# Performance work log

Measured on AMD Instinct MI355X. Metric: run time of the kernel, lower is better.

## Reference

```python
import jax, jax.numpy as jnp
import numpy as np

N, E, IN, H0, H1 = 50000, 1600000, 64, 64, 128


def _gcn(h, W, b, row, col):
    # PyG GCNConv, add_self_loops=False, unit edge weights:
    # out[col] += d^{-1/2}[row] * d^{-1/2}[col] * (h @ W)[row]; bias added after aggregation
    n = h.shape[0]
    deg = jnp.zeros((n,), h.dtype).at[col].add(jnp.ones((row.shape[0],), h.dtype))
    dinv = jnp.where(deg > 0, jax.lax.rsqrt(jnp.maximum(deg, 1e-12)), 0.0)
    norm = (dinv[row] * dinv[col])[:, None]  # [E,1]
    m = h @ W  # transform before propagate (small GEMM)
    out = jnp.zeros((n, W.shape[1]), h.dtype).at[col].add(norm * m[row])
    return out + b


def _bn(h, g, b):
    # BatchNorm1d training-mode math (biased variance), eps=1e-5
    mu = h.mean(0)
    var = ((h - mu) ** 2).mean(0)
    return g * (h - mu) * jax.lax.rsqrt(var + 1e-5) + b


def _san(h):
    return jnp.nan_to_num(h, nan=0.0, posinf=100.0, neginf=-100.0)


def _slice(x, ei, W0, b0, W1, b1, res1, g0, be0, g1, be1):
    row, col = ei[0], ei[1]
    # layer 0: conv -> bn -> relu -> (dropout=eval identity) -> residual (Identity, 64==64) -> nan_to_num
    h1 = _san(jax.nn.relu(_bn(_gcn(x, W0, b0, row, col), g0, be0)) + x)
    # layer 1 (last): conv -> bn -> residual (Linear proj 64->128, no bias) -> nan_to_num
    h2 = _san(_bn(_gcn(h1, W1, b1, row, col), g1, be1) + h1 @ res1)
    return h2


def setup_inputs() -> dict:
    k = jax.random.split(jax.random.key(0), 16)
    f = lambda kk, sh, s: jax.random.normal(kk, sh, jnp.float32) * s
    return {
        "x": f(k[0], (N, IN), 1.0),
        "edge_index0": jax.random.randint(k[1], (2, E), 0, N),
        "edge_index1": jax.random.randint(k[2], (2, E), 0, N),
        "w0_s0": f(k[3], (IN, H0), 0.1), "b0_s0": jnp.zeros((H0,), jnp.float32),
        "w1_s0": f(k[4], (H0, H1), 0.1), "b1_s0": jnp.zeros((H1,), jnp.float32),
        "res1_s0": f(k[5], (H0, H1), 0.1),
        "w0_s1": f(k[6], (IN, H0), 0.1), "b0_s1": jnp.zeros((H0,), jnp.float32),
        "w1_s1": f(k[7], (H0, H1), 0.1), "b1_s1": jnp.zeros((H1,), jnp.float32),
        "res1_s1": f(k[8], (H0, H1), 0.1),
        "bn_g0": jnp.ones((H0,), jnp.float32), "bn_b0": jnp.zeros((H0,), jnp.float32),
        "bn_g1": jnp.ones((H1,), jnp.float32), "bn_b1": jnp.zeros((H1,), jnp.float32),
        "fc1_w": f(k[9], (2 * H1, H1), 0.1), "fc1_b": jnp.zeros((H1,), jnp.float32),
        "fc2_w": f(k[10], (H1, 2), 0.1), "fc2_b": jnp.zeros((2,), jnp.float32),
    }


def reference(x, edge_index0, edge_index1,
              w0_s0, b0_s0, w1_s0, b1_s0, res1_s0,
              w0_s1, b0_s1, w1_s1, b1_s1, res1_s1,
              bn_g0, bn_b0, bn_g1, bn_b1,
              fc1_w, fc1_b, fc2_w, fc2_b):
    out0 = _slice(x, edge_index0, w0_s0, b0_s0, w1_s0, b1_s0, res1_s0, bn_g0, bn_b0, bn_g1, bn_b1)
    out1 = _slice(x, edge_index1, w0_s1, b0_s1, w1_s1, b1_s1, res1_s1, bn_g0, bn_b0, bn_g1, bn_b1)
    combined = jnp.concatenate([out0, out1], axis=1)  # [N, 2*H1]
    h = jax.nn.relu(combined @ fc1_w + fc1_b)  # dropout is eval-mode identity
    logits = h @ fc2_w + fc2_b
    return logits, jax.nn.softmax(logits, axis=1)
```

## Files before the change

kernel.cpp:

```cpp
#include <hip/hip_runtime.h>
#include <hip/hip_bf16.h>
#include <math.h>


typedef short v8s __attribute__((ext_vector_type(8)));
typedef float f32x4 __attribute__((ext_vector_type(4)));

#define BSTRIDE 10240

__device__ __forceinline__ float sanf(float v) {
    if (v != v) return 0.f;
    if (isinf(v)) return v > 0.f ? 100.f : -100.f;
    return v;
}

__device__ __forceinline__ unsigned short bf16of(float v) {
    __hip_bfloat16 h = __float2bfloat16(v);
    return *(unsigned short*)&h;
}
__device__ __forceinline__ unsigned pack2(float lo, float hi) {
    return (unsigned)bf16of(lo) | ((unsigned)bf16of(hi) << 16);
}
__device__ __forceinline__ float uflo(unsigned u) { return __uint_as_float(u << 16); }
__device__ __forceinline__ float ufhi(unsigned u) { return __uint_as_float(u & 0xFFFF0000u); }
__device__ __forceinline__ float fofbf16(unsigned short u) {
    return __uint_as_float(((unsigned)u) << 16);
}

__device__ __forceinline__ void packone(const float* __restrict__ src, unsigned* __restrict__ dst,
                                        int L, int Khalf, int F) {
    int c = L / Khalf, kp = L - c * Khalf;
    dst[L] = pack2(src[(2 * kp) * F + c], src[(2 * kp + 1) * F + c]);
}

__global__ __launch_bounds__(256) void prep_kernel(const float* __restrict__ w0_0,
                                                   const float* __restrict__ w0_1,
                                                   const float* __restrict__ w1_0,
                                                   const float* __restrict__ w1_1,
                                                   const float* __restrict__ r_0,
                                                   const float* __restrict__ r_1,
                                                   const float* __restrict__ fc1,
                                                   unsigned* __restrict__ wpk,
                                                   int* __restrict__ bcnt,
                                                   float* __restrict__ sums) {
    int gid = blockIdx.x * 256 + threadIdx.x;
    if (gid < 512) bcnt[gid] = 0;
    if (gid < 8192) sums[gid] = 0.f;
    if (gid < 2048)       packone(w0_0, wpk + 0,     gid - 0,     32, 64);
    else if (gid < 4096)  packone(w0_1, wpk + 2048,  gid - 2048,  32, 64);
    else if (gid < 8192)  packone(w1_0, wpk + 4096,  gid - 4096,  32, 128);
    else if (gid < 12288) packone(w1_1, wpk + 8192,  gid - 8192,  32, 128);
    else if (gid < 16384) packone(r_0,  wpk + 12288, gid - 12288, 32, 128);
    else if (gid < 20480) packone(r_1,  wpk + 16384, gid - 16384, 32, 128);
    else if (gid < 36864) packone(fc1,  wpk + 20480, gid - 20480, 128, 128);
}


__global__ __launch_bounds__(512) void kC_bin(const int* __restrict__ ei0,
                                              const int* __restrict__ ei1,
                                              int* __restrict__ bcnt,
                                              unsigned* __restrict__ binned,
                                              int E, int n) {
    __shared__ int cnt[512];
    __shared__ int base[512];
    int t = threadIdx.x;
    cnt[t] = 0;
    int E2 = 2 * E;
    int e0 = blockIdx.x * 8192;
    unsigned pk[16];
    int bk[16];
    __syncthreads();
#pragma unroll
    for (int j = 0; j < 16; ++j) {
        int ge = e0 + t + j * 512;
        bk[j] = -1;
        if (ge < E2) {
            int slice = ge >= E;
            const int* ei = slice ? ei1 : ei0;
            int e = ge - slice * E;
            int col = ei[E + e], row = ei[e];
            int gcol = slice * n + col;
            bk[j] = gcol >> 8;
            pk[j] = (unsigned)row | (((unsigned)gcol & 255u) << 16);
            atomicAdd(&cnt[bk[j]], 1);
        }
    }
    __syncthreads();
    {
        int c = cnt[t];
        base[t] = c ? atomicAdd(&bcnt[t], c) : 0;
    }
    __syncthreads();
    cnt[t] = 0;
    __syncthreads();
#pragma unroll
    for (int j = 0; j < 16; ++j) {
        if (bk[j] >= 0) {
            int loc = atomicAdd(&cnt[bk[j]], 1);
            int off = base[bk[j]] + loc;
            if (off < BSTRIDE) binned[(size_t)bk[j] * BSTRIDE + off] = pk[j];
        }
    }
}

__global__ __launch_bounds__(256) void kB_scan(const int* __restrict__ bcnt,
                                               int* __restrict__ bstart, int NB) {
    __shared__ int tmp[256];
    int t = threadIdx.x, carry = 0;
    for (int bse = 0; bse < NB; bse += 256) {
        int i = bse + t;
        int v = (i < NB) ? bcnt[i] : 0;
        tmp[t] = v;
        __syncthreads();
        for (int off = 1; off < 256; off <<= 1) {
            int u = (t >= off) ? tmp[t - off] : 0;
            __syncthreads();
            tmp[t] += u;
            __syncthreads();
        }
        if (i < NB) bstart[i] = tmp[t] - v + carry;
        carry += tmp[255];
        __syncthreads();
    }
    if (t == 0) bstart[NB] = carry;
}

__global__ __launch_bounds__(512) void kD_build(const unsigned* __restrict__ binned,
                                                const int* __restrict__ bstart,
                                                int* __restrict__ rowptr,
                                                float* __restrict__ dinv,
                                                unsigned short* __restrict__ csr,
                                                int n2, int NB) {
    __shared__ int cnt[256];
    __shared__ int scn[256];
    __shared__ int cur[256];
    int b = blockIdx.x, t = threadIdx.x;
    int s = bstart[b], e = bstart[b + 1];
    int m = e - s;
    const unsigned* seg = binned + (size_t)b * BSTRIDE;
    if (t < 256) cnt[t] = 0;
    __syncthreads();
    for (int i = t; i < m; i += 512) atomicAdd(&cnt[(seg[i] >> 16) & 255], 1);
    __syncthreads();
    int v = (t < 256) ? cnt[t] : 0;
    if (t < 256) scn[t] = v;
    __syncthreads();
    for (int off = 1; off < 256; off <<= 1) {
        int u = (t < 256 && t >= off) ? scn[t - off] : 0;
        __syncthreads();
        if (t < 256) scn[t] += u;
        __syncthreads();
    }
    if (t < 256) {
        int excl = scn[t] - v;
        int gcol = b * 256 + t;
        if (gcol < n2) {
            rowptr[gcol] = s + excl;
            dinv[gcol] = v > 0 ? rsqrtf((float)v) : 0.f;
        }
        cur[t] = excl;
    }
    __syncthreads();
    for (int i = t; i < m; i += 512) {
        unsigned p = seg[i];
        int cl = (p >> 16) & 255;
        int pos = s + atomicAdd(&cur[cl], 1);
        csr[pos] = (unsigned short)(p & 0xFFFFu);
    }
    if (b == 0 && t == 0) rowptr[n2] = bstart[NB];
}


__global__ __launch_bounds__(256) void prescale_bf(const float* __restrict__ x,
                                                   const float* __restrict__ dinv,
                                                   unsigned short* __restrict__ xsb,
                                                   int n64, int n) {
    int i = blockIdx.x * 256 + threadIdx.x;
    if (i >= n64) return;
    int row = i >> 6;
    float v = x[i];
    xsb[i] = bf16of(v * dinv[row]);
    xsb[n64 + i] = bf16of(v * dinv[n + row]);
}

__global__ __launch_bounds__(256) void gatherbf_kernel(const int* __restrict__ rowptr,
                                                       const unsigned short* __restrict__ csr,
                                                       const unsigned short* __restrict__ m,
                                                       const float* __restrict__ dinv,
                                                       unsigned short* __restrict__ outb,
                                                       int n, int n2) {
    int gid = blockIdx.x * 256 + threadIdx.x;
    int node = gid >> 3;
    if (node >= n2) return;
    int l = threadIdx.x & 7;
    const unsigned short* mb = m + (size_t)((node >= n) ? n : 0) * 64;
    int s = rowptr[node], e = rowptr[node + 1];
    float a0 = 0.f, a1 = 0.f, a2 = 0.f, a3 = 0.f, a4 = 0.f, a5 = 0.f, a6 = 0.f, a7 = 0.f;
    int b = s;
    for (; b + 8 <= e; b += 8) {
        int idx = csr[b + l];
        uint4 u[8];
#pragma unroll
        for (int j = 0; j < 8; ++j) {
            int r = __shfl(idx, j, 8);
            u[j] = *(const uint4*)&mb[(size_t)r * 64 + l * 8];
        }
#pragma unroll
        for (int j = 0; j < 8; ++j) {
            a0 += uflo(u[j].x); a1 += ufhi(u[j].x);
            a2 += uflo(u[j].y); a3 += ufhi(u[j].y);
            a4 += uflo(u[j].z); a5 += ufhi(u[j].z);
            a6 += uflo(u[j].w); a7 += ufhi(u[j].w);
        }
    }
    if (b < e) {
        int cntn = e - b;
        int idx = (b + l < e) ? (int)csr[b + l] : 0;
        for (int j = 0; j < cntn; ++j) {
            int r = __shfl(idx, j, 8);
            uint4 u = *(const uint4*)&mb[(size_t)r * 64 + l * 8];
            a0 += uflo(u.x); a1 += ufhi(u.x);
            a2 += uflo(u.y); a3 += ufhi(u.y);
            a4 += uflo(u.z); a5 += ufhi(u.z);
            a6 += uflo(u.w); a7 += ufhi(u.w);
        }
    }
    float d = dinv[node];
    uint4 o;
    o.x = pack2(a0 * d, a1 * d);
    o.y = pack2(a2 * d, a3 * d);
    o.z = pack2(a4 * d, a5 * d);
    o.w = pack2(a6 * d, a7 * d);
    *(uint4*)&outb[(size_t)node * 64 + l * 8] = o;
}


template <int F>
__global__ __launch_bounds__(256) void mfma_gemmb(const unsigned short* __restrict__ Ab,
                                                  const unsigned* __restrict__ WT0,
                                                  const unsigned* __restrict__ WT1,
                                                  unsigned short* __restrict__ Cb,
                                                  float* __restrict__ sums_base,
                                                  int roff, int n) {
    constexpr int NC = F / 16;
    __shared__ float ls[2 * F];
    int BPS = (n + 63) >> 6;
    int slice = blockIdx.x >= BPS;
    int sb = blockIdx.x - slice * BPS;
    const unsigned* WT = slice ? WT1 : WT0;
    int row0 = slice * n + sb * 64;
    int rows = min(64, n - sb * 64);
    for (int i = threadIdx.x; i < 2 * F; i += 256) ls[i] = 0.f;
    int w = threadIdx.x >> 6, lane = threadIdx.x & 63, q = lane >> 4, ln = lane & 15;
    const unsigned* A32 = (const unsigned*)Ab;
    size_t arow = (size_t)(row0 + 16 * w + ln) * 32;
    v8s af0 = *(const v8s*)&A32[arow + q * 4];
    v8s af1 = *(const v8s*)&A32[arow + 16 + q * 4];
    f32x4 acc[NC];
#pragma unroll
    for (int ct = 0; ct < NC; ++ct) acc[ct] = {0.f, 0.f, 0.f, 0.f};
#pragma unroll
    for (int ct = 0; ct < NC; ++ct) {
        v8s b0 = *(const v8s*)&WT[(ct * 16 + ln) * 32 + q * 4];
        v8s b1 = *(const v8s*)&WT[(ct * 16 + ln) * 32 + 16 + q * 4];
        acc[ct] = __builtin_amdgcn_mfma_f32_16x16x32_bf16(af0, b0, acc[ct], 0, 0, 0);
        acc[ct] = __builtin_amdgcn_mfma_f32_16x16x32_bf16(af1, b1, acc[ct], 0, 0, 0);
    }
    __syncthreads();
#pragma unroll
    for (int ct = 0; ct < NC; ++ct) {
        float s1 = 0.f, s2 = 0.f;
#pragma unroll
        for (int i = 0; i < 4; ++i) {
            int r = 16 * w + q * 4 + i;
            if (r < rows) {
                float v = acc[ct][i];
                Cb[(size_t)(row0 + r) * F + ct * 16 + ln] = bf16of(v);
                s1 += v;
                s2 += v * v;
            }
        }
        s1 += __shfl_xor(s1, 16); s1 += __shfl_xor(s1, 32);
        s2 += __shfl_xor(s2, 16); s2 += __shfl_xor(s2, 32);
        if (q == 0) {
            atomicAdd(&ls[ct * 16 + ln], s1);
            atomicAdd(&ls[F + ct * 16 + ln], s2);
        }
    }
    __syncthreads();
    if (threadIdx.x < F) {
        float* dst = sums_base + (blockIdx.x & 7) * 1024 + roff + slice * 2 * F;
        unsafeAtomicAdd(&dst[threadIdx.x], ls[threadIdx.x]);
        unsafeAtomicAdd(&dst[F + threadIdx.x], ls[F + threadIdx.x]);
    }
}

__global__ __launch_bounds__(256) void mfma_apply1(const unsigned short* __restrict__ h1b,
                                                   const unsigned short* __restrict__ Tb,
                                                   const unsigned* __restrict__ RT0,
                                                   const unsigned* __restrict__ RT1,
                                                   const float* __restrict__ scsh,
                                                   unsigned short* __restrict__ comb, int n) {
    int BPS = (n + 63) >> 6;
    int slice = blockIdx.x >= BPS;
    int sb = blockIdx.x - slice * BPS;
    const unsigned* WT = slice ? RT1 : RT0;
    int row0 = slice * n + sb * 64;
    int rows = min(64, n - sb * 64);
    int w = threadIdx.x >> 6, lane = threadIdx.x & 63, q = lane >> 4, ln = lane & 15;
    const unsigned* A32 = (const unsigned*)h1b;
    size_t arow = (size_t)(row0 + 16 * w + ln) * 32;
    v8s af0 = *(const v8s*)&A32[arow + q * 4];
    v8s af1 = *(const v8s*)&A32[arow + 16 + q * 4];
    f32x4 acc[8];
#pragma unroll
    for (int ct = 0; ct < 8; ++ct) acc[ct] = {0.f, 0.f, 0.f, 0.f};
#pragma unroll
    for (int ct = 0; ct < 8; ++ct) {
        v8s b0 = *(const v8s*)&WT[(ct * 16 + ln) * 32 + q * 4];
        v8s b1 = *(const v8s*)&WT[(ct * 16 + ln) * 32 + 16 + q * 4];
        acc[ct] = __builtin_amdgcn_mfma_f32_16x16x32_bf16(af0, b0, acc[ct], 0, 0, 0);
        acc[ct] = __builtin_amdgcn_mfma_f32_16x16x32_bf16(af1, b1, acc[ct], 0, 0, 0);
    }
    const float* sc = scsh + slice * 256;
#pragma unroll
    for (int ct = 0; ct < 8; ++ct) {
        int c = ct * 16 + ln;
        float scale = sc[c], shift = sc[128 + c];
#pragma unroll
        for (int i = 0; i < 4; ++i) {
            int r = 16 * w + q * 4 + i;
            if (r >= rows) continue;
            int row = row0 + r;
            float tv = fofbf16(Tb[(size_t)row * 128 + c]);
            float o = sanf(fmaf(tv, scale, shift) + acc[ct][i]);
            comb[(size_t)(row - slice * n) * 256 + slice * 128 + c] = bf16of(o);
        }
    }
}

__global__ __launch_bounds__(256) void mfma_head_fc2(const unsigned short* __restrict__ comb,
                                                     const unsigned* __restrict__ FT,
                                                     const float* __restrict__ bias,
                                                     const float* __restrict__ w2,
                                                     const float* __restrict__ b2,
                                                     float* __restrict__ out, int n) {
    int row0 = blockIdx.x * 64;
    int rows = min(64, n - row0);
    int w = threadIdx.x >> 6, lane = threadIdx.x & 63, q = lane >> 4, ln = lane & 15;
    const unsigned* A32 = (const unsigned*)comb;
    size_t arow = (size_t)(row0 + 16 * w + ln) * 128;
    f32x4 acc[8];
#pragma unroll
    for (int ct = 0; ct < 8; ++ct) acc[ct] = {0.f, 0.f, 0.f, 0.f};
#pragma unroll
    for (int kt = 0; kt < 4; ++kt) {
        v8s af0 = *(const v8s*)&A32[arow + kt * 32 + q * 4];
        v8s af1 = *(const v8s*)&A32[arow + kt * 32 + 16 + q * 4];
#pragma unroll
        for (int ct = 0; ct < 8; ++ct) {
            v8s b0 = *(const v8s*)&FT[(ct * 16 + ln) * 128 + kt * 32 + q * 4];
            v8s b1 = *(const v8s*)&FT[(ct * 16 + ln) * 128 + kt * 32 + 16 + q * 4];
            acc[ct] = __builtin_amdgcn_mfma_f32_16x16x32_bf16(af0, b0, acc[ct], 0, 0, 0);
            acc[ct] = __builtin_amdgcn_mfma_f32_16x16x32_bf16(af1, b1, acc[ct], 0, 0, 0);
        }
    }
    float p0[4] = {0.f, 0.f, 0.f, 0.f}, p1[4] = {0.f, 0.f, 0.f, 0.f};
#pragma unroll
    for (int ct = 0; ct < 8; ++ct) {
        int c = ct * 16 + ln;
        float bi = bias[c];
        float w20 = w2[c * 2], w21 = w2[c * 2 + 1];
#pragma unroll
        for (int i = 0; i < 4; ++i) {
            float h = fmaxf(acc[ct][i] + bi, 0.f);
            p0[i] = fmaf(h, w20, p0[i]);
            p1[i] = fmaf(h, w21, p1[i]);
        }
    }
#pragma unroll
    for (int i = 0; i < 4; ++i) {
#pragma unroll
        for (int msk = 1; msk < 16; msk <<= 1) {
            p0[i] += __shfl_xor(p0[i], msk);
            p1[i] += __shfl_xor(p1[i], msk);
        }
    }
    if (ln == 0) {
        float bb0 = b2[0], bb1 = b2[1];
#pragma unroll
        for (int i = 0; i < 4; ++i) {
            int r = 16 * w + q * 4 + i;
            if (r >= rows) continue;
            int R = row0 + r;
            float l0 = p0[i] + bb0, l1 = p1[i] + bb1;
            float mx = fmaxf(l0, l1);
            float e0 = expf(l0 - mx), e1 = expf(l1 - mx);
            float inv = 1.0f / (e0 + e1);
            out[(size_t)R * 2] = l0;
            out[(size_t)R * 2 + 1] = l1;
            out[(size_t)2 * n + R * 2] = e0 * inv;
            out[(size_t)2 * n + R * 2 + 1] = e1 * inv;
        }
    }
}


template <int F>
__global__ void bnfinal_kernel(const float* __restrict__ sums_base, int roff,
                               const float* __restrict__ g,
                               const float* __restrict__ be, float* __restrict__ scsh, int n) {
    int f = threadIdx.x;
    if (f >= F) return;
    int slice = blockIdx.x;
    float s1 = 0.f, s2 = 0.f;
#pragma unroll
    for (int r = 0; r < 8; ++r) {
        const float* src = sums_base + r * 1024 + roff + slice * 2 * F;
        s1 += src[f];
        s2 += src[F + f];
    }
    float inv_n = 1.0f / (float)n;
    float mu = s1 * inv_n;
    float var = fmaxf(s2 * inv_n - mu * mu, 0.f);
    float scale = g[f] * rsqrtf(var + 1e-5f);
    scsh[slice * 2 * F + f] = scale;
    scsh[slice * 2 * F + F + f] = be[f] - mu * scale;
}

__global__ __launch_bounds__(256) void apply0_kernel(const unsigned short* __restrict__ t0b,
                                                     const float* __restrict__ x,
                                                     const float* __restrict__ scsh,
                                                     const float* __restrict__ dinv,
                                                     unsigned short* __restrict__ h1b,
                                                     unsigned short* __restrict__ h1sb,
                                                     int n64, int total) {
    int i = blockIdx.x * 256 + threadIdx.x;
    if (i >= total) return;
    int slice = i >= n64;
    int f = i & 63;
    const float* sc = scsh + slice * 128;
    float v = fmaf(fofbf16(t0b[i]), sc[f], sc[64 + f]);
    v = fmaxf(v, 0.f) + x[i - slice * n64];
    v = sanf(v);
    h1b[i] = bf16of(v);
    h1sb[i] = bf16of(v * dinv[i >> 6]);
}

static inline int cdiv(int a, int b) { return (a + b - 1) / b; }

extern "C" void kernel_launch(void* const* d_in, const int* in_sizes, int n_in,
                              void* d_out, int out_size, void* d_ws, size_t ws_size,
                              hipStream_t stream) {
    const float* x       = (const float*)d_in[0];
    const int*   ei0     = (const int*)d_in[1];
    const int*   ei1     = (const int*)d_in[2];
    const float* w0_s0   = (const float*)d_in[3];
    const float* w1_s0   = (const float*)d_in[5];
    const float* res1_s0 = (const float*)d_in[7];
    const float* w0_s1   = (const float*)d_in[8];
    const float* w1_s1   = (const float*)d_in[10];
    const float* res1_s1 = (const float*)d_in[12];
    const float* bn_g0   = (const float*)d_in[13];
    const float* bn_b0   = (const float*)d_in[14];
    const float* bn_g1   = (const float*)d_in[15];
    const float* bn_b1   = (const float*)d_in[16];
    const float* fc1_w   = (const float*)d_in[17];
    const float* fc1_b   = (const float*)d_in[18];
    const float* fc2_w   = (const float*)d_in[19];
    const float* fc2_b   = (const float*)d_in[20];
    float* out = (float*)d_out;

    int n = in_sizes[0] / 64;
    int E = in_sizes[1] / 2;
    int n2 = 2 * n, E2 = 2 * E;
    int n64 = n * 64;
    int NB = cdiv(n2, 256);
    int BPS = cdiv(n, 64);

    float* X1 = (float*)d_ws;
    float* S  = X1 + (size_t)n2 * 64;
    unsigned short* Gb   = (unsigned short*)(S + (size_t)n2 * 64);
    unsigned short* h1b  = Gb + (size_t)n2 * 64;
    unsigned short* comb = h1b + (size_t)n2 * 64;
    unsigned short* xsb  = comb + (size_t)n * 256;
    float* dinv = (float*)(xsb + (size_t)n * 128);
    float* sums = dinv + n2;
    float* scsh = sums + 8192;
    unsigned* wpk = (unsigned*)(scsh + 512);
    unsigned short* csr = (unsigned short*)(wpk + 36864);
    int* rowptr = (int*)(csr + (size_t)E2);
    int* bcnt   = rowptr + (n2 + 1);
    int* bstart = bcnt + 512;
    unsigned short* t0b = (unsigned short*)X1;
    unsigned short* Tb  = (unsigned short*)X1;
    unsigned* binned = (unsigned*)comb;
    unsigned short* h1sb = (unsigned short*)S;
    unsigned* w0T0 = wpk + 0,    *w0T1 = wpk + 2048;
    unsigned* w1T0 = wpk + 4096, *w1T1 = wpk + 8192;
    unsigned* rT0  = wpk + 12288,*rT1  = wpk + 16384;
    unsigned* fT   = wpk + 20480;

    prep_kernel<<<144, 256, 0, stream>>>(w0_s0, w0_s1, w1_s0, w1_s1,
                                         res1_s0, res1_s1, fc1_w, wpk, bcnt, sums);
    kC_bin<<<cdiv(E2, 8192), 512, 0, stream>>>(ei0, ei1, bcnt, binned, E, n);
    kB_scan<<<1, 256, 0, stream>>>(bcnt, bstart, NB);
    kD_build<<<NB, 512, 0, stream>>>(binned, bstart, rowptr, dinv, csr, n2, NB);

    prescale_bf<<<cdiv(n64, 256), 256, 0, stream>>>(x, dinv, xsb, n64, n);
    gatherbf_kernel<<<cdiv(n2 * 8, 256), 256, 0, stream>>>(rowptr, csr, xsb, dinv, Gb, n, n2);
    mfma_gemmb<64><<<2 * BPS, 256, 0, stream>>>(Gb, w0T0, w0T1, t0b, sums, 512, n);
    bnfinal_kernel<64><<<2, 64, 0, stream>>>(sums, 512, bn_g0, bn_b0, scsh, n);
    apply0_kernel<<<cdiv(2 * n64, 256), 256, 0, stream>>>(t0b, x, scsh, dinv, h1b, h1sb, n64, 2 * n64);

    gatherbf_kernel<<<cdiv(n2 * 8, 256), 256, 0, stream>>>(rowptr, csr, h1sb, dinv, Gb, n, n2);
    mfma_gemmb<128><<<2 * BPS, 256, 0, stream>>>(Gb, w1T0, w1T1, Tb, sums, 0, n);
    bnfinal_kernel<128><<<2, 128, 0, stream>>>(sums, 0, bn_g1, bn_b1, scsh, n);
    mfma_apply1<<<2 * BPS, 256, 0, stream>>>(h1b, Tb, rT0, rT1, scsh, comb, n);

    mfma_head_fc2<<<BPS, 256, 0, stream>>>(comb, fT, fc1_b, fc2_w, fc2_b, out, n);
}
```

Before: 383.4 us.

## Fuse neighbor gather into MFMA GEMM and fold BN finalize into apply kernels

Fuses the sparse gather-aggregate with the following bf16 MFMA transform, so aggregated rows are staged in LDS instead of round-tripping through global memory. The source-side degree normalization is now applied per edge inside the gather (dinv loaded and shuffled), which removes the prescale kernel and the scaled h1 copy. BatchNorm scale/shift finalization moves into the apply kernels, and the x-to-bf16 conversion is folded into prep. Together these cut launches and intermediate traffic, at the cost of extra per-edge dinv loads and FMAs, and of GEMM blocks that now wait on irregular gather work.

```diff
diff --git a/kernel.cpp b/kernel.cpp
--- a/kernel.cpp
+++ b/kernel.cpp
@@ -40,9 +40,11 @@
                                                    const float* __restrict__ r_0,
                                                    const float* __restrict__ r_1,
                                                    const float* __restrict__ fc1,
+                                                   const float* __restrict__ x,
                                                    unsigned* __restrict__ wpk,
                                                    int* __restrict__ bcnt,
-                                                   float* __restrict__ sums) {
+                                                   float* __restrict__ sums,
+                                                   unsigned short* __restrict__ xb, int n64) {
     int gid = blockIdx.x * 256 + threadIdx.x;
     if (gid < 512) bcnt[gid] = 0;
     if (gid < 8192) sums[gid] = 0.f;
@@ -53,6 +55,7 @@
     else if (gid < 16384) packone(r_0,  wpk + 12288, gid - 12288, 32, 128);
     else if (gid < 20480) packone(r_1,  wpk + 16384, gid - 16384, 32, 128);
     else if (gid < 36864) packone(fc1,  wpk + 20480, gid - 20480, 128, 128);
+    if (gid < n64) xb[gid] = bf16of(x[gid]);
 }
 
 
@@ -170,92 +173,95 @@
     if (b == 0 && t == 0) rowptr[n2] = bstart[NB];
 }
 
-
-__global__ __launch_bounds__(256) void prescale_bf(const float* __restrict__ x,
-                                                   const float* __restrict__ dinv,
-                                                   unsigned short* __restrict__ xsb,
-                                                   int n64, int n) {
-    int i = blockIdx.x * 256 + threadIdx.x;
-    if (i >= n64) return;
-    int row = i >> 6;
-    float v = x[i];
-    xsb[i] = bf16of(v * dinv[row]);
-    xsb[n64 + i] = bf16of(v * dinv[n + row]);
-}
-
-__global__ __launch_bounds__(256) void gatherbf_kernel(const int* __restrict__ rowptr,
-                                                       const unsigned short* __restrict__ csr,
-                                                       const unsigned short* __restrict__ m,
-                                                       const float* __restrict__ dinv,
-                                                       unsigned short* __restrict__ outb,
-                                                       int n, int n2) {
-    int gid = blockIdx.x * 256 + threadIdx.x;
-    int node = gid >> 3;
-    if (node >= n2) return;
-    int l = threadIdx.x & 7;
-    const unsigned short* mb = m + (size_t)((node >= n) ? n : 0) * 64;
-    int s = rowptr[node], e = rowptr[node + 1];
-    float a0 = 0.f, a1 = 0.f, a2 = 0.f, a3 = 0.f, a4 = 0.f, a5 = 0.f, a6 = 0.f, a7 = 0.f;
-    int b = s;
-    for (; b + 8 <= e; b += 8) {
-        int idx = csr[b + l];
-        uint4 u[8];
-#pragma unroll
-        for (int j = 0; j < 8; ++j) {
-            int r = __shfl(idx, j, 8);
-            u[j] = *(const uint4*)&mb[(size_t)r * 64 + l * 8];
-        }
-#pragma unroll
-        for (int j = 0; j < 8; ++j) {
-            a0 += uflo(u[j].x); a1 += ufhi(u[j].x);
-            a2 += uflo(u[j].y); a3 += ufhi(u[j].y);
-            a4 += uflo(u[j].z); a5 += ufhi(u[j].z);
-            a6 += uflo(u[j].w); a7 += ufhi(u[j].w);
-        }
-    }
-    if (b < e) {
-        int cntn = e - b;
-        int idx = (b + l < e) ? (int)csr[b + l] : 0;
-        for (int j = 0; j < cntn; ++j) {
-            int r = __shfl(idx, j, 8);
-            uint4 u = *(const uint4*)&mb[(size_t)r * 64 + l * 8];
-            a0 += uflo(u.x); a1 += ufhi(u.x);
-            a2 += uflo(u.y); a3 += ufhi(u.y);
-            a4 += uflo(u.z); a5 += ufhi(u.z);
-            a6 += uflo(u.w); a7 += ufhi(u.w);
-        }
-    }
-    float d = dinv[node];
-    uint4 o;
-    o.x = pack2(a0 * d, a1 * d);
-    o.y = pack2(a2 * d, a3 * d);
-    o.z = pack2(a4 * d, a5 * d);
-    o.w = pack2(a6 * d, a7 * d);
-    *(uint4*)&outb[(size_t)node * 64 + l * 8] = o;
-}
-
-
 template <int F>
-__global__ __launch_bounds__(256) void mfma_gemmb(const unsigned short* __restrict__ Ab,
-                                                  const unsigned* __restrict__ WT0,
-                                                  const unsigned* __restrict__ WT1,
-                                                  unsigned short* __restrict__ Cb,
-                                                  float* __restrict__ sums_base,
-                                                  int roff, int n) {
+__global__ __launch_bounds__(256) void gg_kernel(const int* __restrict__ rowptr,
+                                                 const unsigned short* __restrict__ csr,
+                                                 const unsigned short* __restrict__ mtab,
+                                                 size_t slice_stride,
+                                                 const float* __restrict__ dinv,
+                                                 const unsigned* __restrict__ WT0,
+                                                 const unsigned* __restrict__ WT1,
+                                                 unsigned short* __restrict__ Cb,
+                                                 float* __restrict__ sums_base,
+                                                 int roff, int n) {
     constexpr int NC = F / 16;
+    __shared__ unsigned As32[64 * 36];
     __shared__ float ls[2 * F];
     int BPS = (n + 63) >> 6;
     int slice = blockIdx.x >= BPS;
     int sb = blockIdx.x - slice * BPS;
-    const unsigned* WT = slice ? WT1 : WT0;
     int row0 = slice * n + sb * 64;
     int rows = min(64, n - sb * 64);
     for (int i = threadIdx.x; i < 2 * F; i += 256) ls[i] = 0.f;
-    int w = threadIdx.x >> 6, lane = threadIdx.x & 63, q = lane >> 4, ln = lane & 15;
-    const unsigned* A32 = (const unsigned*)Ab;
-    size_t arow = (size_t)(row0 + 16 * w + ln) * 32;
-    v8s af0 = *(const v8s*)&A32[arow + q * 4];
-    v8s af1 = *(const v8s*)&A32[arow + 16 + q * 4];
+    int w = threadIdx.x >> 6, lane = threadIdx.x & 63;
+    int l = lane & 7;
+    const unsigned short* mb = mtab + slice_stride * slice;
+    const float* dsrc = dinv + slice * n;
+#pragma unroll
+    for (int p = 0; p < 2; ++p) {
+        int nl = 16 * w + p * 8 + (lane >> 3);
+        float a0 = 0.f, a1 = 0.f, a2 = 0.f, a3 = 0.f, a4 = 0.f, a5 = 0.f, a6 = 0.f, a7 = 0.f;
+        if (nl < rows) {
+            int node = row0 + nl;
+            int s = rowptr[node], e = rowptr[node + 1];
+            int b = s;
+            for (; b + 8 <= e; b += 8) {
+                int idx = csr[b + l];
+                float wsrc = dsrc[idx];
+                uint4 u[8];
+                float ws[8];
+#pragma unroll
+                for (int j = 0; j < 8; ++j) {
+                    int r = __shfl(idx, j, 8);
+                    ws[j] = __shfl(wsrc, j, 8);
+                    u[j] = *(const uint4*)&mb[(size_t)r * 64 + l * 8];
+                }
+#pragma unroll
+                for (int j = 0; j < 8; ++j) {
+                    a0 = fmaf(ws[j], uflo(u[j].x), a0);
+                    a1 = fmaf(ws[j], ufhi(u[j].x), a1);
+                    a2 = fmaf(ws[j], uflo(u[j].y), a2);
+                    a3 = fmaf(ws[j], ufhi(u[j].y), a3);
+                    a4 = fmaf(ws[j], uflo(u[j].z), a4);
+                    a5 = fmaf(ws[j], ufhi(u[j].z), a5);
+                    a6 = fmaf(ws[j], uflo(u[j].w), a6);
+                    a7 = fmaf(ws[j], ufhi(u[j].w), a7);
+                }
+            }
+            if (b < e) {
+                int cntn = e - b;
+                int idx = (b + l < e) ? (int)csr[b + l] : 0;
+                float wsrc = dsrc[idx];
+                for (int j = 0; j < cntn; ++j) {
+                    int r = __shfl(idx, j, 8);
+                    float wj = __shfl(wsrc, j, 8);
+                    uint4 u = *(const uint4*)&mb[(size_t)r * 64 + l * 8];
+                    a0 = fmaf(wj, uflo(u.x), a0);
+                    a1 = fmaf(wj, ufhi(u.x), a1);
+                    a2 = fmaf(wj, uflo(u.y), a2);
+                    a3 = fmaf(wj, ufhi(u.y), a3);
+                    a4 = fmaf(wj, uflo(u.z), a4);
+                    a5 = fmaf(wj, ufhi(u.z), a5);
+                    a6 = fmaf(wj, uflo(u.w), a6);
+                    a7 = fmaf(wj, ufhi(u.w), a7);
+                }
+            }
+            float d = dinv[node];
+            a0 *= d; a1 *= d; a2 *= d; a3 *= d;
+            a4 *= d; a5 *= d; a6 *= d; a7 *= d;
+        }
+        uint4 o;
+        o.x = pack2(a0, a1);
+        o.y = pack2(a2, a3);
+        o.z = pack2(a4, a5);
+        o.w = pack2(a6, a7);
+        *(uint4*)&As32[nl * 36 + l * 4] = o;
+    }
+    __syncthreads();
+    const unsigned* WT = slice ? WT1 : WT0;
+    int q = lane >> 4, ln = lane & 15;
+    v8s af0 = *(const v8s*)&As32[(16 * w + ln) * 36 + q * 4];
+    v8s af1 = *(const v8s*)&As32[(16 * w + ln) * 36 + 16 + q * 4];
     f32x4 acc[NC];
 #pragma unroll
     for (int ct = 0; ct < NC; ++ct) acc[ct] = {0.f, 0.f, 0.f, 0.f};
@@ -266,7 +272,6 @@
         acc[ct] = __builtin_amdgcn_mfma_f32_16x16x32_bf16(af0, b0, acc[ct], 0, 0, 0);
         acc[ct] = __builtin_amdgcn_mfma_f32_16x16x32_bf16(af1, b1, acc[ct], 0, 0, 0);
     }
-    __syncthreads();
 #pragma unroll
     for (int ct = 0; ct < NC; ++ct) {
         float s1 = 0.f, s2 = 0.f;
@@ -295,19 +300,75 @@
     }
 }
 
+
+__global__ __launch_bounds__(256) void apply0_kernel(const unsigned short* __restrict__ t0b,
+                                                     const float* __restrict__ x,
+                                                     const float* __restrict__ sums_base,
+                                                     int roff,
+                                                     const float* __restrict__ g,
+                                                     const float* __restrict__ be,
+                                                     unsigned short* __restrict__ h1b,
+                                                     int n64, int n) {
+    __shared__ float sc[128];
+    int i0 = blockIdx.x * 256;
+    int slice = i0 >= n64;
+    int t = threadIdx.x;
+    if (t < 64) {
+        float s1 = 0.f, s2 = 0.f;
+#pragma unroll
+        for (int r = 0; r < 8; ++r) {
+            const float* src = sums_base + r * 1024 + roff + slice * 128;
+            s1 += src[t];
+            s2 += src[64 + t];
+        }
+        float inv_n = 1.0f / (float)n;
+        float mu = s1 * inv_n;
+        float var = fmaxf(s2 * inv_n - mu * mu, 0.f);
+        float scale = g[t] * rsqrtf(var + 1e-5f);
+        sc[t] = scale;
+        sc[64 + t] = be[t] - mu * scale;
+    }
+    __syncthreads();
+    int i = i0 + t;
+    int f = i & 63;
+    float v = fmaf(fofbf16(t0b[i]), sc[f], sc[64 + f]);
+    v = fmaxf(v, 0.f) + x[i - slice * n64];
+    h1b[i] = bf16of(sanf(v));
+}
+
 __global__ __launch_bounds__(256) void mfma_apply1(const unsigned short* __restrict__ h1b,
                                                    const unsigned short* __restrict__ Tb,
                                                    const unsigned* __restrict__ RT0,
                                                    const unsigned* __restrict__ RT1,
-                                                   const float* __restrict__ scsh,
+                                                   const float* __restrict__ sums_base,
+                                                   const float* __restrict__ g,
+                                                   const float* __restrict__ be,
                                                    unsigned short* __restrict__ comb, int n) {
+    __shared__ float sc[256];
     int BPS = (n + 63) >> 6;
     int slice = blockIdx.x >= BPS;
     int sb = blockIdx.x - slice * BPS;
-    const unsigned* WT = slice ? RT1 : RT0;
     int row0 = slice * n + sb * 64;
     int rows = min(64, n - sb * 64);
-    int w = threadIdx.x >> 6, lane = threadIdx.x & 63, q = lane >> 4, ln = lane & 15;
+    int t = threadIdx.x;
+    if (t < 128) {
+        float s1 = 0.f, s2 = 0.f;
+#pragma unroll
+        for (int r = 0; r < 8; ++r) {
+            const float* src = sums_base + r * 1024 + slice * 256;
+            s1 += src[t];
+            s2 += src[128 + t];
+        }
+        float inv_n = 1.0f / (float)n;
+        float mu = s1 * inv_n;
+        float var = fmaxf(s2 * inv_n - mu * mu, 0.f);
+        float scale = g[t] * rsqrtf(var + 1e-5f);
+        sc[t] = scale;
+        sc[128 + t] = be[t] - mu * scale;
+    }
+    __syncthreads();
+    const unsigned* WT = slice ? RT1 : RT0;
+    int w = t >> 6, lane = t & 63, q = lane >> 4, ln = lane & 15;
     const unsigned* A32 = (const unsigned*)h1b;
     size_t arow = (size_t)(row0 + 16 * w + ln) * 32;
     v8s af0 = *(const v8s*)&A32[arow + q * 4];
@@ -322,7 +383,6 @@
         acc[ct] = __builtin_amdgcn_mfma_f32_16x16x32_bf16(af0, b0, acc[ct], 0, 0, 0);
         acc[ct] = __builtin_amdgcn_mfma_f32_16x16x32_bf16(af1, b1, acc[ct], 0, 0, 0);
     }
-    const float* sc = scsh + slice * 256;
 #pragma unroll
     for (int ct = 0; ct < 8; ++ct) {
         int c = ct * 16 + ln;
@@ -403,48 +463,6 @@
             out[(size_t)2 * n + R * 2 + 1] = e1 * inv;
         }
     }
-}
-
-
-template <int F>
-__global__ void bnfinal_kernel(const float* __restrict__ sums_base, int roff,
-                               const float* __restrict__ g,
-                               const float* __restrict__ be, float* __restrict__ scsh, int n) {
-    int f = threadIdx.x;
-    if (f >= F) return;
-    int slice = blockIdx.x;
-    float s1 = 0.f, s2 = 0.f;
-#pragma unroll
-    for (int r = 0; r < 8; ++r) {
-        const float* src = sums_base + r * 1024 + roff + slice * 2 * F;
-        s1 += src[f];
-        s2 += src[F + f];
-    }
-    float inv_n = 1.0f / (float)n;
-    float mu = s1 * inv_n;
-    float var = fmaxf(s2 * inv_n - mu * mu, 0.f);
-    float scale = g[f] * rsqrtf(var + 1e-5f);
-    scsh[slice * 2 * F + f] = scale;
-    scsh[slice * 2 * F + F + f] = be[f] - mu * scale;
-}
-
-__global__ __launch_bounds__(256) void apply0_kernel(const unsigned short* __restrict__ t0b,
-                                                     const float* __restrict__ x,
-                                                     const float* __restrict__ scsh,
-                                                     const float* __restrict__ dinv,
-                                                     unsigned short* __restrict__ h1b,
-                                                     unsigned short* __restrict__ h1sb,
-                                                     int n64, int total) {
-    int i = blockIdx.x * 256 + threadIdx.x;
-    if (i >= total) return;
-    int slice = i >= n64;
-    int f = i & 63;
-    const float* sc = scsh + slice * 128;
-    float v = fmaf(fofbf16(t0b[i]), sc[f], sc[64 + f]);
-    v = fmaxf(v, 0.f) + x[i - slice * n64];
-    v = sanf(v);
-    h1b[i] = bf16of(v);
-    h1sb[i] = bf16of(v * dinv[i >> 6]);
 }
 
 static inline int cdiv(int a, int b) { return (a + b - 1) / b; }
@@ -478,45 +496,40 @@
     int NB = cdiv(n2, 256);
     int BPS = cdiv(n, 64);
 
-    float* X1 = (float*)d_ws;
-    float* S  = X1 + (size_t)n2 * 64;
-    unsigned short* Gb   = (unsigned short*)(S + (size_t)n2 * 64);
-    unsigned short* h1b  = Gb + (size_t)n2 * 64;
+    unsigned short* Tb   = (unsigned short*)d_ws;
+    unsigned short* h1b  = Tb + (size_t)n2 * 128;
     unsigned short* comb = h1b + (size_t)n2 * 64;
-    unsigned short* xsb  = comb + (size_t)n * 256;
-    float* dinv = (float*)(xsb + (size_t)n * 128);
+    unsigned short* xb   = comb + (size_t)n * 256;
+    float* dinv = (float*)(xb + (size_t)n * 64);
     float* sums = dinv + n2;
-    float* scsh = sums + 8192;
-    unsigned* wpk = (unsigned*)(scsh + 512);
+    unsigned* wpk = (unsigned*)(sums + 8192);
     unsigned short* csr = (unsigned short*)(wpk + 36864);
     int* rowptr = (int*)(csr + (size_t)E2);
     int* bcnt   = rowptr + (n2 + 1);
     int* bstart = bcnt + 512;
-    unsigned short* t0b = (unsigned short*)X1;
-    unsigned short* Tb  = (unsigned short*)X1;
+    unsigned short* t0b = Tb;
     unsigned* binned = (unsigned*)comb;
-    unsigned short* h1sb = (unsigned short*)S;
     unsigned* w0T0 = wpk + 0,    *w0T1 = wpk + 2048;
     unsigned* w1T0 = wpk + 4096, *w1T1 = wpk + 8192;
     unsigned* rT0  = wpk + 12288,*rT1  = wpk + 16384;
     unsigned* fT   = wpk + 20480;
 
-    prep_kernel<<<144, 256, 0, stream>>>(w0_s0, w0_s1, w1_s0, w1_s1,
-                                         res1_s0, res1_s1, fc1_w, wpk, bcnt, sums);
+    prep_kernel<<<cdiv(n64, 256), 256, 0, stream>>>(w0_s0, w0_s1, w1_s0, w1_s1,
+                                                    res1_s0, res1_s1, fc1_w, x,
+                                                    wpk, bcnt, sums, xb, n64);
     kC_bin<<<cdiv(E2, 8192), 512, 0, stream>>>(ei0, ei1, bcnt, binned, E, n);
     kB_scan<<<1, 256, 0, stream>>>(bcnt, bstart, NB);
     kD_build<<<NB, 512, 0, stream>>>(binned, bstart, rowptr, dinv, csr, n2, NB);
 
-    prescale_bf<<<cdiv(n64, 256), 256, 0, stream>>>(x, dinv, xsb, n64, n);
-    gatherbf_kernel<<<cdiv(n2 * 8, 256), 256, 0, stream>>>(rowptr, csr, xsb, dinv, Gb, n, n2);
-    mfma_gemmb<64><<<2 * BPS, 256, 0, stream>>>(Gb, w0T0, w0T1, t0b, sums, 512, n);
-    bnfinal_kernel<64><<<2, 64, 0, stream>>>(sums, 512, bn_g0, bn_b0, scsh, n);
-    apply0_kernel<<<cdiv(2 * n64, 256), 256, 0, stream>>>(t0b, x, scsh, dinv, h1b, h1sb, n64, 2 * n64);
-
-    gatherbf_kernel<<<cdiv(n2 * 8, 256), 256, 0, stream>>>(rowptr, csr, h1sb, dinv, Gb, n, n2);
-    mfma_gemmb<128><<<2 * BPS, 256, 0, stream>>>(Gb, w1T0, w1T1, Tb, sums, 0, n);
-    bnfinal_kernel<128><<<2, 128, 0, stream>>>(sums, 0, bn_g1, bn_b1, scsh, n);
-    mfma_apply1<<<2 * BPS, 256, 0, stream>>>(h1b, Tb, rT0, rT1, scsh, comb, n);
+    gg_kernel<64><<<2 * BPS, 256, 0, stream>>>(rowptr, csr, xb, 0, dinv,
+                                               w0T0, w0T1, t0b, sums, 512, n);
+    apply0_kernel<<<2 * n64 / 256, 256, 0, stream>>>(t0b, x, sums, 512, bn_g0, bn_b0,
+                                                     h1b, n64, n);
+
+    gg_kernel<128><<<2 * BPS, 256, 0, stream>>>(rowptr, csr, h1b, (size_t)n * 64, dinv,
+                                                w1T0, w1T1, Tb, sums, 0, n);
+    mfma_apply1<<<2 * BPS, 256, 0, stream>>>(h1b, Tb, rT0, rT1, sums, bn_g1, bn_b1,
+                                             comb, n);
 
     mfma_head_fc2<<<BPS, 256, 0, stream>>>(comb, fT, fc1_b, fc2_w, fc2_b, out, n);
 }
```

After: 408.3 us. +6.5%, slower.
